# Optimization experiments

Hardware: AMD Instinct MI355X
Metric: run time of the kernel (lower is better)

## Reference

```python
import jax, jax.numpy as jnp
import numpy as np

NE, NPROC, E, D = 50000, 25000, 200000, 128
L, T = 3, 4  # layers, edge types: 0:e->e, 1:e->p, 2:p->p, 3:p->e


def setup_inputs() -> dict:
    key = jax.random.key(0)
    ks = jax.random.split(key, 17)
    s = 1.0 / np.sqrt(D)
    return {
        'x_elem': jax.random.normal(ks[0], (NE, D), jnp.float32),
        'x_proc': jax.random.normal(ks[1], (NPROC, D), jnp.float32),
        'W_src': jax.random.normal(ks[2], (L, T, D, D), jnp.float32) * s,
        'W_dst': jax.random.normal(ks[3], (L, T, D, D), jnp.float32) * s,
        'att_src': jax.random.normal(ks[4], (L, T, D), jnp.float32) * s,
        'att_dst': jax.random.normal(ks[5], (L, T, D), jnp.float32) * s,
        'bias': jax.random.normal(ks[6], (L, T, D), jnp.float32) * 0.01,
        'lin_W': jax.random.normal(ks[7], (D, 2), jnp.float32) * s,
        'lin_b': jnp.zeros((2,), jnp.float32),
        'ee_src': jax.random.randint(ks[8], (E,), 0, NE),
        'ee_dst': jax.random.randint(ks[9], (E,), 0, NE),
        'ep_src': jax.random.randint(ks[10], (E,), 0, NE),
        'ep_dst': jax.random.randint(ks[11], (E,), 0, NPROC),
        'pp_src': jax.random.randint(ks[12], (E,), 0, NPROC),
        'pp_dst': jax.random.randint(ks[13], (E,), 0, NPROC),
        'pe_src': jax.random.randint(ks[14], (E,), 0, NPROC),
        'pe_dst': jax.random.randint(ks[15], (E,), 0, NE),
    }


def _gat(x_s, x_d, src, dst, n_dst, Ws, Wd, a_s, a_d, b):
    # one GATConv (heads=1, negative_slope=0 -> relu, no self loops)
    hs = x_s @ Ws                       # [Ns, D]
    hd = x_d @ Wd                       # [Nd, D]
    es = hs @ a_s                       # [Ns]
    ed = hd @ a_d                       # [Nd]
    logit = jax.nn.relu(es[src] + ed[dst])              # [E]
    m = jax.ops.segment_max(logit, dst, num_segments=n_dst)
    m = jnp.where(jnp.isfinite(m), m, 0.0)              # empty segments
    w = jnp.exp(logit - m[dst])
    denom = jax.ops.segment_sum(w, dst, num_segments=n_dst)
    alpha = w / jnp.maximum(denom[dst], 1e-16)          # edge softmax per dst
    out = jax.ops.segment_sum(alpha[:, None] * hs[src], dst, num_segments=n_dst)
    return out + b


def reference(x_elem, x_proc, W_src, W_dst, att_src, att_dst, bias, lin_W, lin_b,
              ee_src, ee_dst, ep_src, ep_dst, pp_src, pp_dst, pe_src, pe_dst):
    xe, xp = x_elem, x_proc
    for l in range(L):
        ee = _gat(xe, xe, ee_src, ee_dst, NE, W_src[l, 0], W_dst[l, 0], att_src[l, 0], att_dst[l, 0], bias[l, 0])
        ep = _gat(xe, xp, ep_src, ep_dst, NPROC, W_src[l, 1], W_dst[l, 1], att_src[l, 1], att_dst[l, 1], bias[l, 1])
        pp = _gat(xp, xp, pp_src, pp_dst, NPROC, W_src[l, 2], W_dst[l, 2], att_src[l, 2], att_dst[l, 2], bias[l, 2])
        pe = _gat(xp, xe, pe_src, pe_dst, NE, W_src[l, 3], W_dst[l, 3], att_src[l, 3], att_dst[l, 3], bias[l, 3])
        xe = ee + pe   # to_hetero aggr='sum' per destination node type
        xp = ep + pp
    x = jnp.concatenate([xe, xp], axis=0) @ lin_W + lin_b  # G_aggr
    return x.mean(axis=0)  # [2]
```

## Files before the change

kernel.cpp:

```cpp
#include <hip/hip_runtime.h>

#define NE_N 50000
#define NP_N 25000
#define E_N 200000
#define DIM 128
#define LOG2E 1.4426950408889634f
#define NREP 1024

typedef __attribute__((ext_vector_type(8))) short short8;
typedef __attribute__((ext_vector_type(4))) float f32x4;

static __device__ __forceinline__ ushort f2bf(float f) {
  unsigned x = __float_as_uint(f);
  return (ushort)((x + 0x7fffu + ((x >> 16) & 1u)) >> 16);
}
static __device__ __forceinline__ float bf2f(ushort u) {
  return __uint_as_float(((unsigned)u) << 16);
}

#define SU_CW 12
#define SU_V 6
#define SU_H 3128
__global__ __launch_bounds__(256) void setup_fused(
    const float* __restrict__ W_src, const float* __restrict__ W_dst,
    const float* __restrict__ att_dst, ushort* __restrict__ WbT,
    float* __restrict__ vec, const int* __restrict__ d0,
    const int* __restrict__ d1, const int* __restrict__ d2,
    const int* __restrict__ d3, int* __restrict__ c0, int* __restrict__ c1,
    int* __restrict__ c2, int* __restrict__ c3, ushort* __restrict__ rk0,
    ushort* __restrict__ rk1, ushort* __restrict__ rk2,
    ushort* __restrict__ rk3) {
  int blk = blockIdx.x;
  int tid = threadIdx.x;
  if (blk < SU_CW) {
    const float* src = W_src + (size_t)blk * DIM * DIM;
    ushort* dst = WbT + (size_t)blk * DIM * DIM;
    for (int i = tid; i < DIM * DIM; i += 256) {
      int k = i >> 7, n = i & 127;
      dst[n * DIM + k] = f2bf(src[i]);
    }
  } else if (blk < SU_CW + SU_V) {
    int b = blk - SU_CW;
    int lt = b * 2 + (tid >> 7);
    int i = tid & 127;
    const float* Wd = W_dst + (size_t)lt * DIM * DIM;
    const float* ad = att_dst + lt * DIM;
    float s = 0.f;
#pragma unroll 8
    for (int j = 0; j < DIM; j++) s += Wd[i * DIM + j] * ad[j];
    vec[lt * DIM + i] = s;
  } else {
    int b = blk - SU_CW - SU_V;
    int ty = b / 782;
    int e = (b % 782) * 256 + tid;
    if (e >= E_N) return;
    const int* dst = ty == 0 ? d0 : ty == 1 ? d1 : ty == 2 ? d2 : d3;
    int* cnt = ty == 0 ? c0 : ty == 1 ? c1 : ty == 2 ? c2 : c3;
    ushort* rk = ty == 0 ? rk0 : ty == 1 ? rk1 : ty == 2 ? rk2 : rk3;
    rk[e] = (ushort)atomicAdd(&cnt[dst[e]], 1);
  }
}

__global__ __launch_bounds__(256) void scanA_k(
    const int* __restrict__ c0, const int* __restrict__ c1,
    const int* __restrict__ c2, const int* __restrict__ c3,
    int* __restrict__ part) {
  int ty = blockIdx.y;
  const int* cnt = ty == 0 ? c0 : ty == 1 ? c1 : ty == 2 ? c2 : c3;
  int n = (ty == 0 || ty == 3) ? NE_N : NP_N;
  int nblk = (n + 1023) >> 10;
  if ((int)blockIdx.x >= nblk) return;
  int base = blockIdx.x * 1024 + threadIdx.x * 4;
  int s = 0;
#pragma unroll
  for (int j = 0; j < 4; j++) s += (base + j < n) ? cnt[base + j] : 0;
  int lane = threadIdx.x & 63, wid = threadIdx.x >> 6;
#pragma unroll
  for (int off = 32; off > 0; off >>= 1) s += __shfl_xor(s, off, 64);
  __shared__ int ws4[4];
  if (lane == 0) ws4[wid] = s;
  __syncthreads();
  if (threadIdx.x == 0)
    part[ty * 64 + blockIdx.x] = ws4[0] + ws4[1] + ws4[2] + ws4[3];
}

__global__ __launch_bounds__(256) void scanBC_k(
    const int* __restrict__ c0, const int* __restrict__ c1,
    const int* __restrict__ c2, const int* __restrict__ c3,
    int* __restrict__ r0, int* __restrict__ r1, int* __restrict__ r2,
    int* __restrict__ r3, const int* __restrict__ part) {
  int ty = blockIdx.y;
  int bx = blockIdx.x;
  const int* cnt = ty == 0 ? c0 : ty == 1 ? c1 : ty == 2 ? c2 : c3;
  int* rp = ty == 0 ? r0 : ty == 1 ? r1 : ty == 2 ? r2 : r3;
  int n = (ty == 0 || ty == 3) ? NE_N : NP_N;
  int nblk = (n + 1023) >> 10;
  if (bx >= nblk) return;

  __shared__ int s_excl;
  if (threadIdx.x < 64) {
    int pl = threadIdx.x;
    int v = (pl < nblk) ? part[ty * 64 + pl] : 0;
    int sc = v;
#pragma unroll
    for (int off = 1; off < 64; off <<= 1) {
      int t = __shfl_up(sc, off, 64);
      if (pl >= off) sc += t;
    }
    if (pl == bx) s_excl = sc - v;
  }
  if (bx == 0 && threadIdx.x == 0) rp[n] = E_N;
  __syncthreads();

  int base = bx * 1024 + threadIdx.x * 4;
  int v[4];
#pragma unroll
  for (int j = 0; j < 4; j++) v[j] = (base + j < n) ? cnt[base + j] : 0;
  int s = v[0] + v[1] + v[2] + v[3];
  int lane = threadIdx.x & 63, wid = threadIdx.x >> 6;
  int sc = s;
#pragma unroll
  for (int off = 1; off < 64; off <<= 1) {
    int t = __shfl_up(sc, off, 64);
    if (lane >= off) sc += t;
  }
  __shared__ int ws4[4];
  if (lane == 63) ws4[wid] = sc;
  __syncthreads();
  int wbase = 0;
  for (int w = 0; w < wid; w++) wbase += ws4[w];
  int p = s_excl + wbase + sc - s;
#pragma unroll
  for (int j = 0; j < 4; j++) {
    if (base + j < n) rp[base + j] = p;
    p += v[j];
  }
}

#define EBLK ((NE_N + 127) / 128)
#define PBLK ((NP_N + 127) / 128)
#define GEMM_BLK (EBLK + PBLK)
#define FILL_BLK ((E_N + 511) / 512)

template <bool FP32>
static __device__ __forceinline__ void gemm_body(
    int blk, const void* __restrict__ xev, const void* __restrict__ xpv,
    const ushort* __restrict__ WbT, const float* __restrict__ att,
    const float* __restrict__ vec, int l, unsigned char* __restrict__ hsE0,
    unsigned char* __restrict__ hsE1, unsigned char* __restrict__ hsP3,
    unsigned char* __restrict__ hsP2, float* __restrict__ esE0,
    float* __restrict__ esE1, float* __restrict__ esP3,
    float* __restrict__ esP2, float* __restrict__ edEA,
    float* __restrict__ edEB, float* __restrict__ edPA,
    float* __restrict__ edPB) {
  const void* xb;
  const ushort *W0T, *W1T;
  const float *a0, *a1, *dv0, *dv1;
  unsigned char *hs0, *hs1;
  float *es0, *es1, *edA, *edB;
  int N, rbase;
  if (blk < EBLK) {
    xb = xev; N = NE_N; rbase = blk * 128;
    W0T = WbT + (size_t)(l * 4 + 0) * DIM * DIM;
    W1T = WbT + (size_t)(l * 4 + 1) * DIM * DIM;
    a0 = att + (l * 4 + 0) * DIM; a1 = att + (l * 4 + 1) * DIM;
    dv0 = vec + (l * 4 + 0) * DIM; dv1 = vec + (l * 4 + 3) * DIM;
    hs0 = hsE0; hs1 = hsE1; es0 = esE0; es1 = esE1;
    edA = edEA; edB = edEB;
  } else {
    blk -= EBLK; xb = xpv; N = NP_N; rbase = blk * 128;
    W0T = WbT + (size_t)(l * 4 + 3) * DIM * DIM;
    W1T = WbT + (size_t)(l * 4 + 2) * DIM * DIM;
    a0 = att + (l * 4 + 3) * DIM; a1 = att + (l * 4 + 2) * DIM;
    dv0 = vec + (l * 4 + 1) * DIM; dv1 = vec + (l * 4 + 2) * DIM;
    hs0 = hsP3; hs1 = hsP2; es0 = esP3; es1 = esP2;
    edA = edPA; edB = edPB;
  }

  const int wave = threadIdx.x >> 6;
  const int lane = threadIdx.x & 63;
  const int m = lane & 15, quad = lane >> 4;
  const int row0 = rbase + wave * 16;
  int rowA = row0 + m;
  if (rowA >= N) rowA = N - 1;

  float4 xraw[8];
  short8 xvv[4];
  if (FP32) {
    const float* xf32 = (const float*)xb + (size_t)rowA * DIM + quad * 8;
#pragma unroll
    for (int k0 = 0; k0 < 4; k0++) {
      xraw[2 * k0] = *(const float4*)(xf32 + k0 * 32);
      xraw[2 * k0 + 1] = *(const float4*)(xf32 + k0 * 32 + 4);
    }
  } else {
    const ushort* xb16 = (const ushort*)xb + (size_t)rowA * DIM + quad * 8;
#pragma unroll
    for (int k0 = 0; k0 < 4; k0++)
      xvv[k0] = *(const short8*)(xb16 + k0 * 32);
  }

  __shared__ short8 wlds[4096];
  {
    const int i15 = lane & 15, i4 = lane >> 4;
#pragma unroll
    for (int r = 0; r < 8; r++) {
      const int g = r * 8 + wave;
      const int set = g >> 5, k0 = (g >> 3) & 3, f = g & 7;
      const ushort* WT = set ? W1T : W0T;
      wlds[g * 64 + lane] = *(const short8*)(
          WT + (size_t)(f * 16 + i15) * DIM + k0 * 32 + i4 * 8);
    }
  }
  __syncthreads();
  if (row0 >= N) return;

  float edp0 = 0.f, edp1 = 0.f;
#pragma unroll
  for (int k0 = 0; k0 < 4; k0++) {
    float xf[8];
    if (FP32) {
      float4 f0 = xraw[2 * k0], f1 = xraw[2 * k0 + 1];
      xf[0] = f0.x; xf[1] = f0.y; xf[2] = f0.z; xf[3] = f0.w;
      xf[4] = f1.x; xf[5] = f1.y; xf[6] = f1.z; xf[7] = f1.w;
      short8 xv;
#pragma unroll
      for (int j = 0; j < 8; j++) xv[j] = (short)f2bf(xf[j]);
      xvv[k0] = xv;
    } else {
#pragma unroll
      for (int j = 0; j < 8; j++) xf[j] = bf2f((ushort)xvv[k0][j]);
    }
    int off = k0 * 32 + quad * 8;
    float4 vA0 = *(const float4*)&dv0[off];
    float4 vA1 = *(const float4*)&dv0[off + 4];
    float4 vB0 = *(const float4*)&dv1[off];
    float4 vB1 = *(const float4*)&dv1[off + 4];
    edp0 += xf[0] * vA0.x + xf[1] * vA0.y + xf[2] * vA0.z + xf[3] * vA0.w +
            xf[4] * vA1.x + xf[5] * vA1.y + xf[6] * vA1.z + xf[7] * vA1.w;
    edp1 += xf[0] * vB0.x + xf[1] * vB0.y + xf[2] * vB0.z + xf[3] * vB0.w +
            xf[4] * vB1.x + xf[5] * vB1.y + xf[6] * vB1.z + xf[7] * vB1.w;
  }

  f32x4 acc0[8], acc1[8];
#pragma unroll
  for (int f = 0; f < 8; f++) {
    acc0[f] = (f32x4){0.f, 0.f, 0.f, 0.f};
    acc1[f] = (f32x4){0.f, 0.f, 0.f, 0.f};
  }
#pragma unroll
  for (int k0 = 0; k0 < 4; k0++) {
    const short8 xv = xvv[k0];
#pragma unroll
    for (int f = 0; f < 8; f++) {
      acc0[f] = __builtin_amdgcn_mfma_f32_16x16x32_bf16(
          wlds[(k0 * 8 + f) * 64 + lane], xv, acc0[f], 0, 0, 0);
      acc1[f] = __builtin_amdgcn_mfma_f32_16x16x32_bf16(
          wlds[2048 + (k0 * 8 + f) * 64 + lane], xv, acc1[f], 0, 0, 0);
    }
  }

  const int row = row0 + m;
  edp0 += __shfl_xor(edp0, 16, 64);
  edp0 += __shfl_xor(edp0, 32, 64);
  edp1 += __shfl_xor(edp1, 16, 64);
  edp1 += __shfl_xor(edp1, 32, 64);
  if (quad == 0 && row < N) {
    edA[row] = edp0 * LOG2E;
    edB[row] = edp1 * LOG2E;
  }

#pragma unroll
  for (int set = 0; set < 2; set++) {
    f32x4* acc = set ? acc1 : acc0;
    const float* as = set ? a1 : a0;
    float* es = set ? es1 : es0;
    unsigned char* hs = set ? hs1 : hs0;

    float esum = 0.f;
#pragma unroll
    for (int f = 0; f < 8; f++) {
      float4 av = *(const float4*)&as[f * 16 + quad * 4];
      esum += acc[f][0] * av.x + acc[f][1] * av.y + acc[f][2] * av.z +
              acc[f][3] * av.w;
    }
    esum += __shfl_xor(esum, 16, 64);
    esum += __shfl_xor(esum, 32, 64);
    if (quad == 0 && row < N) es[row] = esum * LOG2E;

    if (row < N) {
#pragma unroll
      for (int f = 0; f < 8; f++) {
        int w = __builtin_amdgcn_cvt_pk_fp8_f32(acc[f][0], acc[f][1], 0, false);
        w = __builtin_amdgcn_cvt_pk_fp8_f32(acc[f][2], acc[f][3], w, true);
        *(unsigned*)&hs[(size_t)row * DIM + f * 16 + quad * 4] = (unsigned)w;
      }
    }
  }
}

__global__ __launch_bounds__(512, 4) void gemm_k(
    const ushort* __restrict__ xe, const ushort* __restrict__ xp,
    const ushort* __restrict__ WbT, const float* __restrict__ att,
    const float* __restrict__ vec, int l, unsigned char* __restrict__ hsE0,
    unsigned char* __restrict__ hsE1, unsigned char* __restrict__ hsP3,
    unsigned char* __restrict__ hsP2, float* __restrict__ esE0,
    float* __restrict__ esE1, float* __restrict__ esP3,
    float* __restrict__ esP2, float* __restrict__ edEA,
    float* __restrict__ edEB, float* __restrict__ edPA,
    float* __restrict__ edPB) {
  gemm_body<false>(blockIdx.x, xe, xp, WbT, att, vec, l, hsE0, hsE1, hsP3,
                   hsP2, esE0, esE1, esP3, esP2, edEA, edEB, edPA, edPB);
}

__global__ __launch_bounds__(512, 4) void fill_gemm0_k(
    const float* __restrict__ xe, const float* __restrict__ xp,
    const ushort* __restrict__ WbT, const float* __restrict__ att,
    const float* __restrict__ vec, unsigned char* __restrict__ hsE0,
    unsigned char* __restrict__ hsE1, unsigned char* __restrict__ hsP3,
    unsigned char* __restrict__ hsP2, float* __restrict__ esE0,
    float* __restrict__ esE1, float* __restrict__ esP3,
    float* __restrict__ esP2, float* __restrict__ edEA,
    float* __restrict__ edEB, float* __restrict__ edPA,
    float* __restrict__ edPB, const int* __restrict__ s0,
    const int* __restrict__ s1, const int* __restrict__ s2,
    const int* __restrict__ s3, const int* __restrict__ d0,
    const int* __restrict__ d1, const int* __restrict__ d2,
    const int* __restrict__ d3, const ushort* __restrict__ rk0,
    const ushort* __restrict__ rk1, const ushort* __restrict__ rk2,
    const ushort* __restrict__ rk3, const int* __restrict__ r0,
    const int* __restrict__ r1, const int* __restrict__ r2,
    const int* __restrict__ r3, ushort* __restrict__ o0,
    ushort* __restrict__ o1, ushort* __restrict__ o2,
    ushort* __restrict__ o3) {
  int blk = blockIdx.x;
  if (blk < GEMM_BLK) {
    gemm_body<true>(blk, xe, xp, WbT, att, vec, 0, hsE0, hsE1, hsP3, hsP2,
                    esE0, esE1, esP3, esP2, edEA, edEB, edPA, edPB);
  } else {
    int b = blk - GEMM_BLK;
    int ty = b / FILL_BLK;
    int e = (b % FILL_BLK) * 512 + threadIdx.x;
    if (e >= E_N) return;
    const int* src = ty == 0 ? s0 : ty == 1 ? s1 : ty == 2 ? s2 : s3;
    const int* dst = ty == 0 ? d0 : ty == 1 ? d1 : ty == 2 ? d2 : d3;
    const ushort* rk = ty == 0 ? rk0 : ty == 1 ? rk1 : ty == 2 ? rk2 : rk3;
    const int* rp = ty == 0 ? r0 : ty == 1 ? r1 : ty == 2 ? r2 : r3;
    ushort* out = ty == 0 ? o0 : ty == 1 ? o1 : ty == 2 ? o2 : o3;
    out[rp[dst[e]] + rk[e]] = (ushort)src[e];
  }
}

__global__ __launch_bounds__(256) void gat_gather_all(
    const int* __restrict__ rp0, const ushort* __restrict__ ss0,
    const int* __restrict__ rp1, const ushort* __restrict__ ss1,
    const int* __restrict__ rp2, const ushort* __restrict__ ss2,
    const int* __restrict__ rp3, const ushort* __restrict__ ss3,
    const float* __restrict__ esE0, const unsigned char* __restrict__ hsE0,
    const float* __restrict__ esE1, const unsigned char* __restrict__ hsE1,
    const float* __restrict__ esP3, const unsigned char* __restrict__ hsP3,
    const float* __restrict__ esP2, const unsigned char* __restrict__ hsP2,
    const float* __restrict__ edEA, const float* __restrict__ edEB,
    const float* __restrict__ edPA, const float* __restrict__ edPB,
    const float* __restrict__ bias, int l, ushort* __restrict__ outxe,
    ushort* __restrict__ outxp, int to_csum, float* __restrict__ csum_rep) {
  const int wid = (blockIdx.x * 256 + threadIdx.x) >> 6;
  const int lane = threadIdx.x & 63;
  const int slot = lane >> 3, sub = lane & 7;
  const int half = slot >> 2;
  const int hslot = slot & 3;
  const bool active = wid < NE_N + NP_N;

  float v0 = 0.f, v1 = 0.f;
  const float *b0 = bias, *b1 = bias;
  ushort* outb = outxe;
  int node = 0;

  if (active) {
    const int *rpA, *rpB;
    const ushort *ssA, *ssB;
    const float *esA, *esB;
    const unsigned char *hsA, *hsB;
    const float *edA, *edB;
    if (wid < NE_N) {
      node = wid;
      rpA = rp0; ssA = ss0; esA = esE0; hsA = hsE0;
      rpB = rp3; ssB = ss3; esB = esP3; hsB = hsP3;
      edA = edEA; edB = edEB;
      b0 = bias + (l * 4 + 0) * DIM; b1 = bias + (l * 4 + 3) * DIM;
      outb = outxe;
    } else {
      node = wid - NE_N;
      rpA = rp1; ssA = ss1; esA = esE1; hsA = hsE1;
      rpB = rp2; ssB = ss2; esB = esP2; hsB = hsP2;
      edA = edPA; edB = edPB;
      b0 = bias + (l * 4 + 1) * DIM; b1 = bias + (l * 4 + 2) * DIM;
      outb = outxp;
    }

    const int* rp = half ? rpB : rpA;
    const ushort* ss = half ? ssB : ssA;
    const float* es = half ? esB : esA;
    const unsigned char* hs = half ? hsB : hsA;
    const float edv = half ? edB[node] : edA[node];
    const int beg = rp[node], end = rp[node + 1];

    float acc[16];
#pragma unroll
    for (int j = 0; j < 16; j++) acc[j] = 0.f;
    float sw = 0.f;

    for (int e = beg + hslot; e < end; e += 4) {
      int s = ss[e];
      float w = exp2f(fmaxf(es[s] + edv, 0.f));
      sw += w;
      uint4 h = *(const uint4*)&hs[(size_t)s * DIM + sub * 16];
      auto p0 = __builtin_amdgcn_cvt_pk_f32_fp8((int)h.x, false);
      auto p1 = __builtin_amdgcn_cvt_pk_f32_fp8((int)h.x, true);
      auto p2 = __builtin_amdgcn_cvt_pk_f32_fp8((int)h.y, false);
      auto p3 = __builtin_amdgcn_cvt_pk_f32_fp8((int)h.y, true);
      auto p4 = __builtin_amdgcn_cvt_pk_f32_fp8((int)h.z, false);
      auto p5 = __builtin_amdgcn_cvt_pk_f32_fp8((int)h.z, true);
      auto p6 = __builtin_amdgcn_cvt_pk_f32_fp8((int)h.w, false);
      auto p7 = __builtin_amdgcn_cvt_pk_f32_fp8((int)h.w, true);
      acc[0] += w * p0[0];  acc[1] += w * p0[1];
      acc[2] += w * p1[0];  acc[3] += w * p1[1];
      acc[4] += w * p2[0];  acc[5] += w * p2[1];
      acc[6] += w * p3[0];  acc[7] += w * p3[1];
      acc[8] += w * p4[0];  acc[9] += w * p4[1];
      acc[10] += w * p5[0]; acc[11] += w * p5[1];
      acc[12] += w * p6[0]; acc[13] += w * p6[1];
      acc[14] += w * p7[0]; acc[15] += w * p7[1];
    }

    sw += __shfl_xor(sw, 8, 64);
    sw += __shfl_xor(sw, 16, 64);
    const float inv = 1.f / fmaxf(sw, 1e-16f);

    float res[16];
#pragma unroll
    for (int j = 0; j < 16; j++) res[j] = acc[j] * inv;

#pragma unroll
    for (int j = 0; j < 16; j++) {
      res[j] += __shfl_xor(res[j], 8, 64);
      res[j] += __shfl_xor(res[j], 16, 64);
      res[j] += __shfl_xor(res[j], 32, 64);
    }
    v0 = res[slot * 2];
    v1 = res[slot * 2 + 1];
  }

  const int d = sub * 16 + slot * 2;
  if (to_csum) {
    __shared__ float lsum[4][DIM];
    const int wv = threadIdx.x >> 6;
    lsum[wv][d] = v0;
    lsum[wv][d + 1] = v1;
    __syncthreads();
    if (threadIdx.x < DIM) {
      float s = lsum[0][threadIdx.x] + lsum[1][threadIdx.x] +
                lsum[2][threadIdx.x] + lsum[3][threadIdx.x];
      float* rep = csum_rep + (size_t)(blockIdx.x & (NREP - 1)) * DIM;
      unsafeAtomicAdd(&rep[threadIdx.x], s);
    }
  } else if (active) {
    float2 bb0 = *(const float2*)&b0[d];
    float2 bb1 = *(const float2*)&b1[d];
    ushort2 o;
    o.x = f2bf(v0 + bb0.x + bb1.x);
    o.y = f2bf(v1 + bb0.y + bb1.y);
    *(ushort2*)&outb[(size_t)node * DIM + d] = o;
  }
}

__global__ __launch_bounds__(512) void final_proj(
    const float* __restrict__ csum_rep, const float* __restrict__ bias,
    const float* __restrict__ lin_W, const float* __restrict__ lin_b,
    float* __restrict__ out) {
  __shared__ float parts[4][DIM];
  __shared__ float col[DIM];
  const int k = threadIdx.x & 127;
  const int pt = threadIdx.x >> 7;
  float s = 0.f;
#pragma unroll 8
  for (int r = pt * (NREP / 4); r < (pt + 1) * (NREP / 4); r++)
    s += csum_rep[(size_t)r * DIM + k];
  parts[pt][k] = s;
  __syncthreads();
  if (threadIdx.x < DIM) {
    const float* bE0 = bias + (2 * 4 + 0) * DIM;
    const float* bE1 = bias + (2 * 4 + 3) * DIM;
    const float* bP0 = bias + (2 * 4 + 1) * DIM;
    const float* bP1 = bias + (2 * 4 + 2) * DIM;
    col[k] = parts[0][k] + parts[1][k] + parts[2][k] + parts[3][k] +
             (float)NE_N * (bE0[k] + bE1[k]) +
             (float)NP_N * (bP0[k] + bP1[k]);
  }
  __syncthreads();
  if (threadIdx.x < 2) {
    float acc = 0.f;
#pragma unroll 8
    for (int j = 0; j < DIM; j++) acc += col[j] * lin_W[j * 2 + threadIdx.x];
    out[threadIdx.x] = acc / (float)(NE_N + NP_N) + lin_b[threadIdx.x];
  }
}

extern "C" void kernel_launch(void* const* d_in, const int* in_sizes, int n_in,
                              void* d_out, int out_size, void* d_ws,
                              size_t ws_size, hipStream_t stream) {
  const float* x_elem  = (const float*)d_in[0];
  const float* x_proc  = (const float*)d_in[1];
  const float* W_src   = (const float*)d_in[2];
  const float* W_dst   = (const float*)d_in[3];
  const float* att_src = (const float*)d_in[4];
  const float* att_dst = (const float*)d_in[5];
  const float* bias    = (const float*)d_in[6];
  const float* lin_W   = (const float*)d_in[7];
  const float* lin_b   = (const float*)d_in[8];
  const int* esrc[4] = {(const int*)d_in[9],  (const int*)d_in[11],
                        (const int*)d_in[13], (const int*)d_in[15]};
  const int* edst[4] = {(const int*)d_in[10], (const int*)d_in[12],
                        (const int*)d_in[14], (const int*)d_in[16]};

  char* p = (char*)d_ws;
  ushort* xe_bf[2]; ushort* xp_bf[2];
  xe_bf[0] = (ushort*)p; p += (size_t)NE_N * DIM * 2;
  xe_bf[1] = (ushort*)p; p += (size_t)NE_N * DIM * 2;
  xp_bf[0] = (ushort*)p; p += (size_t)NP_N * DIM * 2;
  xp_bf[1] = (ushort*)p; p += (size_t)NP_N * DIM * 2;
  unsigned char* hsE0 = (unsigned char*)p; p += (size_t)NE_N * DIM;
  unsigned char* hsE1 = (unsigned char*)p; p += (size_t)NE_N * DIM;
  unsigned char* hsP3 = (unsigned char*)p; p += (size_t)NP_N * DIM;
  unsigned char* hsP2 = (unsigned char*)p; p += (size_t)NP_N * DIM;
  ushort* WbT = (ushort*)p; p += (size_t)12 * DIM * DIM * 2;
  float* esE0 = (float*)p; p += (size_t)NE_N * 4;
  float* esE1 = (float*)p; p += (size_t)NE_N * 4;
  float* esP3 = (float*)p; p += (size_t)NP_N * 4;
  float* esP2 = (float*)p; p += (size_t)NP_N * 4;
  float* edEA = (float*)p; p += (size_t)NE_N * 4;
  float* edEB = (float*)p; p += (size_t)NE_N * 4;
  float* edPA = (float*)p; p += (size_t)NP_N * 4;
  float* edPB = (float*)p; p += (size_t)NP_N * 4;
  float* vec = (float*)p; p += 12 * DIM * 4;
  int* parti = (int*)p; p += 4 * 64 * 4;
  int* cnt[4];
  for (int t = 0; t < 4; t++) { cnt[t] = (int*)p; p += (NE_N + 4) * 4; }
  float* csum_rep = (float*)p; p += (size_t)NREP * DIM * 4;
  int* rp[4];
  for (int t = 0; t < 4; t++) { rp[t] = (int*)p; p += (NE_N + 4) * 4; }
  ushort* ssrc[4];
  for (int t = 0; t < 4; t++) { ssrc[t] = (ushort*)p; p += (size_t)E_N * 2; }
  ushort* rank[4];
  for (int t = 0; t < 4; t++) { rank[t] = (ushort*)p; p += (size_t)E_N * 2; }

  hipMemsetAsync(cnt[0], 0,
                 4 * (NE_N + 4) * sizeof(int) + (size_t)NREP * DIM * sizeof(float),
                 stream);

  setup_fused<<<SU_CW + SU_V + SU_H, 256, 0, stream>>>(
      W_src, W_dst, att_dst, WbT, vec, edst[0], edst[1], edst[2], edst[3],
      cnt[0], cnt[1], cnt[2], cnt[3], rank[0], rank[1], rank[2], rank[3]);

  scanA_k<<<dim3(49, 4), 256, 0, stream>>>(cnt[0], cnt[1], cnt[2], cnt[3],
                                           parti);
  scanBC_k<<<dim3(49, 4), 256, 0, stream>>>(cnt[0], cnt[1], cnt[2], cnt[3],
                                            rp[0], rp[1], rp[2], rp[3], parti);

  fill_gemm0_k<<<GEMM_BLK + 4 * FILL_BLK, 512, 0, stream>>>(
      x_elem, x_proc, WbT, att_src, vec, hsE0, hsE1, hsP3, hsP2, esE0, esE1,
      esP3, esP2, edEA, edEB, edPA, edPB, esrc[0], esrc[1], esrc[2], esrc[3],
      edst[0], edst[1], edst[2], edst[3], rank[0], rank[1], rank[2], rank[3],
      rp[0], rp[1], rp[2], rp[3], ssrc[0], ssrc[1], ssrc[2], ssrc[3]);

  int c = 0;
  for (int l = 0; l < 3; l++) {
    if (l > 0) {
      gemm_k<<<GEMM_BLK, 512, 0, stream>>>(
          xe_bf[c], xp_bf[c], WbT, att_src, vec, l, hsE0, hsE1, hsP3, hsP2,
          esE0, esE1, esP3, esP2, edEA, edEB, edPA, edPB);
    }
    int to_csum = (l == 2) ? 1 : 0;
    gat_gather_all<<<(NE_N + NP_N) / 4, 256, 0, stream>>>(
        rp[0], ssrc[0], rp[1], ssrc[1], rp[2], ssrc[2], rp[3], ssrc[3], esE0,
        hsE0, esE1, hsE1, esP3, hsP3, esP2, hsP2, edEA, edEB, edPA, edPB,
        bias, l, xe_bf[1 - c], xp_bf[1 - c], to_csum, csum_rep);
    c = 1 - c;
  }

  final_proj<<<1, 512, 0, stream>>>(csum_rep, bias, lin_W, lin_b,
                                    (float*)d_out);
}
```

Measured before the change: 412.4 us.

## Overlap layer-0 GEMM with edge histogram, interleave blocks, split fill kernel

Moves the atomic degree-histogram and rank computation out of the setup kernel and into the layer-0 GEMM launch, so the GEMM and the histogram run concurrently. Histogram blocks are spread evenly among GEMM blocks by proportional index mapping, which mixes compute-bound and atomic-bound blocks on the GPU. The CSR fill becomes its own small kernel after the scans. The setup kernel now only handles weight conversion, and the GEMM0 output no longer waits on the scans. The cost is one extra launch.

```diff
diff --git a/kernel.cpp b/kernel.cpp
--- a/kernel.cpp
+++ b/kernel.cpp
@@ -20,16 +20,10 @@
 
 #define SU_CW 12
 #define SU_V 6
-#define SU_H 3128
-__global__ __launch_bounds__(256) void setup_fused(
+__global__ __launch_bounds__(256) void setup_w(
     const float* __restrict__ W_src, const float* __restrict__ W_dst,
     const float* __restrict__ att_dst, ushort* __restrict__ WbT,
-    float* __restrict__ vec, const int* __restrict__ d0,
-    const int* __restrict__ d1, const int* __restrict__ d2,
-    const int* __restrict__ d3, int* __restrict__ c0, int* __restrict__ c1,
-    int* __restrict__ c2, int* __restrict__ c3, ushort* __restrict__ rk0,
-    ushort* __restrict__ rk1, ushort* __restrict__ rk2,
-    ushort* __restrict__ rk3) {
+    float* __restrict__ vec) {
   int blk = blockIdx.x;
   int tid = threadIdx.x;
   if (blk < SU_CW) {
@@ -39,7 +33,7 @@
       int k = i >> 7, n = i & 127;
       dst[n * DIM + k] = f2bf(src[i]);
     }
-  } else if (blk < SU_CW + SU_V) {
+  } else {
     int b = blk - SU_CW;
     int lt = b * 2 + (tid >> 7);
     int i = tid & 127;
@@ -49,15 +43,6 @@
 #pragma unroll 8
     for (int j = 0; j < DIM; j++) s += Wd[i * DIM + j] * ad[j];
     vec[lt * DIM + i] = s;
-  } else {
-    int b = blk - SU_CW - SU_V;
-    int ty = b / 782;
-    int e = (b % 782) * 256 + tid;
-    if (e >= E_N) return;
-    const int* dst = ty == 0 ? d0 : ty == 1 ? d1 : ty == 2 ? d2 : d3;
-    int* cnt = ty == 0 ? c0 : ty == 1 ? c1 : ty == 2 ? c2 : c3;
-    ushort* rk = ty == 0 ? rk0 : ty == 1 ? rk1 : ty == 2 ? rk2 : rk3;
-    rk[e] = (ushort)atomicAdd(&cnt[dst[e]], 1);
   }
 }
 
@@ -140,7 +125,8 @@
 #define EBLK ((NE_N + 127) / 128)
 #define PBLK ((NP_N + 127) / 128)
 #define GEMM_BLK (EBLK + PBLK)
-#define FILL_BLK ((E_N + 511) / 512)
+#define HIST_BLK ((E_N + 511) / 512)
+#define HG_TOT (GEMM_BLK + 4 * HIST_BLK)
 
 template <bool FP32>
 static __device__ __forceinline__ void gemm_body(
@@ -313,7 +299,7 @@
                    hsP2, esE0, esE1, esP3, esP2, edEA, edEB, edPA, edPB);
 }
 
-__global__ __launch_bounds__(512, 4) void fill_gemm0_k(
+__global__ __launch_bounds__(512, 4) void hist_gemm0_k(
     const float* __restrict__ xe, const float* __restrict__ xp,
     const ushort* __restrict__ WbT, const float* __restrict__ att,
     const float* __restrict__ vec, unsigned char* __restrict__ hsE0,
@@ -322,33 +308,51 @@
     float* __restrict__ esE1, float* __restrict__ esP3,
     float* __restrict__ esP2, float* __restrict__ edEA,
     float* __restrict__ edEB, float* __restrict__ edPA,
-    float* __restrict__ edPB, const int* __restrict__ s0,
-    const int* __restrict__ s1, const int* __restrict__ s2,
-    const int* __restrict__ s3, const int* __restrict__ d0,
+    float* __restrict__ edPB, const int* __restrict__ d0,
     const int* __restrict__ d1, const int* __restrict__ d2,
-    const int* __restrict__ d3, const ushort* __restrict__ rk0,
-    const ushort* __restrict__ rk1, const ushort* __restrict__ rk2,
-    const ushort* __restrict__ rk3, const int* __restrict__ r0,
-    const int* __restrict__ r1, const int* __restrict__ r2,
-    const int* __restrict__ r3, ushort* __restrict__ o0,
-    ushort* __restrict__ o1, ushort* __restrict__ o2,
-    ushort* __restrict__ o3) {
-  int blk = blockIdx.x;
-  if (blk < GEMM_BLK) {
-    gemm_body<true>(blk, xe, xp, WbT, att, vec, 0, hsE0, hsE1, hsP3, hsP2,
+    const int* __restrict__ d3, int* __restrict__ c0, int* __restrict__ c1,
+    int* __restrict__ c2, int* __restrict__ c3, ushort* __restrict__ rk0,
+    ushort* __restrict__ rk1, ushort* __restrict__ rk2,
+    ushort* __restrict__ rk3) {
+  const int blk = blockIdx.x;
+  const int q0 = (blk * GEMM_BLK) / HG_TOT;
+  const int q1 = ((blk + 1) * GEMM_BLK) / HG_TOT;
+  if (q1 > q0) {
+    gemm_body<true>(q0, xe, xp, WbT, att, vec, 0, hsE0, hsE1, hsP3, hsP2,
                     esE0, esE1, esP3, esP2, edEA, edEB, edPA, edPB);
   } else {
-    int b = blk - GEMM_BLK;
-    int ty = b / FILL_BLK;
-    int e = (b % FILL_BLK) * 512 + threadIdx.x;
+    const int hb = blk - q0;
+    const int ty = hb / HIST_BLK;
+    const int e = (hb % HIST_BLK) * 512 + threadIdx.x;
     if (e >= E_N) return;
-    const int* src = ty == 0 ? s0 : ty == 1 ? s1 : ty == 2 ? s2 : s3;
     const int* dst = ty == 0 ? d0 : ty == 1 ? d1 : ty == 2 ? d2 : d3;
-    const ushort* rk = ty == 0 ? rk0 : ty == 1 ? rk1 : ty == 2 ? rk2 : rk3;
-    const int* rp = ty == 0 ? r0 : ty == 1 ? r1 : ty == 2 ? r2 : r3;
-    ushort* out = ty == 0 ? o0 : ty == 1 ? o1 : ty == 2 ? o2 : o3;
-    out[rp[dst[e]] + rk[e]] = (ushort)src[e];
-  }
+    int* cnt = ty == 0 ? c0 : ty == 1 ? c1 : ty == 2 ? c2 : c3;
+    ushort* rk = ty == 0 ? rk0 : ty == 1 ? rk1 : ty == 2 ? rk2 : rk3;
+    rk[e] = (ushort)atomicAdd(&cnt[dst[e]], 1);
+  }
+}
+
+__global__ __launch_bounds__(512) void fill_k(
+    const int* __restrict__ s0, const int* __restrict__ s1,
+    const int* __restrict__ s2, const int* __restrict__ s3,
+    const int* __restrict__ d0, const int* __restrict__ d1,
+    const int* __restrict__ d2, const int* __restrict__ d3,
+    const ushort* __restrict__ rk0, const ushort* __restrict__ rk1,
+    const ushort* __restrict__ rk2, const ushort* __restrict__ rk3,
+    const int* __restrict__ r0, const int* __restrict__ r1,
+    const int* __restrict__ r2, const int* __restrict__ r3,
+    ushort* __restrict__ o0, ushort* __restrict__ o1,
+    ushort* __restrict__ o2, ushort* __restrict__ o3) {
+  int b = blockIdx.x;
+  int ty = b / HIST_BLK;
+  int e = (b % HIST_BLK) * 512 + threadIdx.x;
+  if (e >= E_N) return;
+  const int* src = ty == 0 ? s0 : ty == 1 ? s1 : ty == 2 ? s2 : s3;
+  const int* dst = ty == 0 ? d0 : ty == 1 ? d1 : ty == 2 ? d2 : d3;
+  const ushort* rk = ty == 0 ? rk0 : ty == 1 ? rk1 : ty == 2 ? rk2 : rk3;
+  const int* rp = ty == 0 ? r0 : ty == 1 ? r1 : ty == 2 ? r2 : r3;
+  ushort* out = ty == 0 ? o0 : ty == 1 ? o1 : ty == 2 ? o2 : o3;
+  out[rp[dst[e]] + rk[e]] = (ushort)src[e];
 }
 
 __global__ __launch_bounds__(256) void gat_gather_all(
@@ -558,8 +562,11 @@
                  4 * (NE_N + 4) * sizeof(int) + (size_t)NREP * DIM * sizeof(float),
                  stream);
 
-  setup_fused<<<SU_CW + SU_V + SU_H, 256, 0, stream>>>(
-      W_src, W_dst, att_dst, WbT, vec, edst[0], edst[1], edst[2], edst[3],
+  setup_w<<<SU_CW + SU_V, 256, 0, stream>>>(W_src, W_dst, att_dst, WbT, vec);
+
+  hist_gemm0_k<<<HG_TOT, 512, 0, stream>>>(
+      x_elem, x_proc, WbT, att_src, vec, hsE0, hsE1, hsP3, hsP2, esE0, esE1,
+      esP3, esP2, edEA, edEB, edPA, edPB, edst[0], edst[1], edst[2], edst[3],
       cnt[0], cnt[1], cnt[2], cnt[3], rank[0], rank[1], rank[2], rank[3]);
 
   scanA_k<<<dim3(49, 4), 256, 0, stream>>>(cnt[0], cnt[1], cnt[2], cnt[3],
@@ -567,11 +574,10 @@
   scanBC_k<<<dim3(49, 4), 256, 0, stream>>>(cnt[0], cnt[1], cnt[2], cnt[3],
                                             rp[0], rp[1], rp[2], rp[3], parti);
 
-  fill_gemm0_k<<<GEMM_BLK + 4 * FILL_BLK, 512, 0, stream>>>(
-      x_elem, x_proc, WbT, att_src, vec, hsE0, hsE1, hsP3, hsP2, esE0, esE1,
-      esP3, esP2, edEA, edEB, edPA, edPB, esrc[0], esrc[1], esrc[2], esrc[3],
-      edst[0], edst[1], edst[2], edst[3], rank[0], rank[1], rank[2], rank[3],
-      rp[0], rp[1], rp[2], rp[3], ssrc[0], ssrc[1], ssrc[2], ssrc[3]);
+  fill_k<<<4 * HIST_BLK, 512, 0, stream>>>(
+      esrc[0], esrc[1], esrc[2], esrc[3], edst[0], edst[1], edst[2], edst[3],
+      rank[0], rank[1], rank[2], rank[3], rp[0], rp[1], rp[2], rp[3],
+      ssrc[0], ssrc[1], ssrc[2], ssrc[3]);
 
   int c = 0;
   for (int l = 0; l < 3; l++) {
```

Result: no change. 410.6 us (-0.4%).

## Replace global atomic degree counting with chunked LDS hash histograms

Applied to the files above, without the earlier changes.

Each of 32 edge chunks per edge type now counts destination degrees in a shared-memory open-addressing hash table, writing local ranks and a per-node, per-chunk count table. The first scan kernel prefix-sums each node's 32 chunk counts in place to obtain totals. The fill step adds the chunk offset to the row pointer and local rank. Fill and GEMM blocks in the fused kernel are also interleaved rather than placed back to back. The goal is to remove contended global atomics, at the cost of a 32-entry-per-node count table (extra memset and scan traffic) and hash-probe work in LDS.

```diff
diff --git a/kernel.cpp b/kernel.cpp
--- a/kernel.cpp
+++ b/kernel.cpp
@@ -7,6 +7,10 @@
 #define LOG2E 1.4426950408889634f
 #define NREP 1024
 
+#define NCHK 32
+#define CHK_E (E_N / NCHK)
+#define TBL 16384
+
 typedef __attribute__((ext_vector_type(8))) short short8;
 typedef __attribute__((ext_vector_type(4))) float f32x4;
 
@@ -18,62 +22,102 @@
   return __uint_as_float(((unsigned)u) << 16);
 }
 
-#define SU_CW 12
-#define SU_V 6
-#define SU_H 3128
-__global__ __launch_bounds__(256) void setup_fused(
+#define HIST_BLKS (4 * NCHK)
+#define HS_TOT (HIST_BLKS + 12 + 3)
+__global__ __launch_bounds__(512) void hist_setup_k(
     const float* __restrict__ W_src, const float* __restrict__ W_dst,
     const float* __restrict__ att_dst, ushort* __restrict__ WbT,
     float* __restrict__ vec, const int* __restrict__ d0,
     const int* __restrict__ d1, const int* __restrict__ d2,
-    const int* __restrict__ d3, int* __restrict__ c0, int* __restrict__ c1,
-    int* __restrict__ c2, int* __restrict__ c3, ushort* __restrict__ rk0,
+    const int* __restrict__ d3, ushort* __restrict__ h0,
+    ushort* __restrict__ h1, ushort* __restrict__ h2,
+    ushort* __restrict__ h3, ushort* __restrict__ rk0,
     ushort* __restrict__ rk1, ushort* __restrict__ rk2,
     ushort* __restrict__ rk3) {
-  int blk = blockIdx.x;
-  int tid = threadIdx.x;
-  if (blk < SU_CW) {
-    const float* src = W_src + (size_t)blk * DIM * DIM;
-    ushort* dst = WbT + (size_t)blk * DIM * DIM;
-    for (int i = tid; i < DIM * DIM; i += 256) {
+  __shared__ int keys[TBL];
+  __shared__ int cnts[TBL];
+  const int blk = blockIdx.x;
+  const int tid = threadIdx.x;
+  if (blk < HIST_BLKS) {
+    const int ty = blk >> 5, c = blk & (NCHK - 1);
+    const int* dst = ty == 0 ? d0 : ty == 1 ? d1 : ty == 2 ? d2 : d3;
+    ushort* h = ty == 0 ? h0 : ty == 1 ? h1 : ty == 2 ? h2 : h3;
+    ushort* rk = ty == 0 ? rk0 : ty == 1 ? rk1 : ty == 2 ? rk2 : rk3;
+    for (int i = tid; i < TBL; i += 512) { keys[i] = -1; cnts[i] = 0; }
+    __syncthreads();
+    const int base = c * CHK_E;
+    for (int i = tid; i < CHK_E; i += 512) {
+      const int e = base + i;
+      const int d = dst[e];
+      unsigned hsh = ((unsigned)d * 2654435761u) >> 18;
+      hsh &= (TBL - 1);
+      int lr;
+      while (true) {
+        int prev = atomicCAS(&keys[hsh], -1, d);
+        if (prev == -1 || prev == d) { lr = atomicAdd(&cnts[hsh], 1); break; }
+        hsh = (hsh + 1) & (TBL - 1);
+      }
+      rk[e] = (ushort)lr;
+    }
+    __syncthreads();
+    for (int i = tid; i < TBL; i += 512) {
+      int k = keys[i];
+      if (k >= 0) h[(size_t)k * NCHK + c] = (ushort)cnts[i];
+    }
+  } else if (blk < HIST_BLKS + 12) {
+    const int w = blk - HIST_BLKS;
+    const float* src = W_src + (size_t)w * DIM * DIM;
+    ushort* dstw = WbT + (size_t)w * DIM * DIM;
+    for (int i = tid; i < DIM * DIM; i += 512) {
       int k = i >> 7, n = i & 127;
-      dst[n * DIM + k] = f2bf(src[i]);
-    }
-  } else if (blk < SU_CW + SU_V) {
-    int b = blk - SU_CW;
-    int lt = b * 2 + (tid >> 7);
-    int i = tid & 127;
+      dstw[n * DIM + k] = f2bf(src[i]);
+    }
+  } else {
+    const int b = blk - HIST_BLKS - 12;
+    const int lt = b * 4 + (tid >> 7);
+    const int i = tid & 127;
     const float* Wd = W_dst + (size_t)lt * DIM * DIM;
     const float* ad = att_dst + lt * DIM;
     float s = 0.f;
 #pragma unroll 8
     for (int j = 0; j < DIM; j++) s += Wd[i * DIM + j] * ad[j];
     vec[lt * DIM + i] = s;
-  } else {
-    int b = blk - SU_CW - SU_V;
-    int ty = b / 782;
-    int e = (b % 782) * 256 + tid;
-    if (e >= E_N) return;
-    const int* dst = ty == 0 ? d0 : ty == 1 ? d1 : ty == 2 ? d2 : d3;
-    int* cnt = ty == 0 ? c0 : ty == 1 ? c1 : ty == 2 ? c2 : c3;
-    ushort* rk = ty == 0 ? rk0 : ty == 1 ? rk1 : ty == 2 ? rk2 : rk3;
-    rk[e] = (ushort)atomicAdd(&cnt[dst[e]], 1);
   }
 }
 
 __global__ __launch_bounds__(256) void scanA_k(
-    const int* __restrict__ c0, const int* __restrict__ c1,
-    const int* __restrict__ c2, const int* __restrict__ c3,
+    ushort* __restrict__ h0, ushort* __restrict__ h1,
+    ushort* __restrict__ h2, ushort* __restrict__ h3, int* __restrict__ c0,
+    int* __restrict__ c1, int* __restrict__ c2, int* __restrict__ c3,
     int* __restrict__ part) {
   int ty = blockIdx.y;
-  const int* cnt = ty == 0 ? c0 : ty == 1 ? c1 : ty == 2 ? c2 : c3;
+  ushort* h = ty == 0 ? h0 : ty == 1 ? h1 : ty == 2 ? h2 : h3;
+  int* cnt = ty == 0 ? c0 : ty == 1 ? c1 : ty == 2 ? c2 : c3;
   int n = (ty == 0 || ty == 3) ? NE_N : NP_N;
   int nblk = (n + 1023) >> 10;
   if ((int)blockIdx.x >= nblk) return;
   int base = blockIdx.x * 1024 + threadIdx.x * 4;
   int s = 0;
 #pragma unroll
-  for (int j = 0; j < 4; j++) s += (base + j < n) ? cnt[base + j] : 0;
+  for (int j = 0; j < 4; j++) {
+    int node = base + j;
+    if (node < n) {
+      uint4* hp = (uint4*)(h + (size_t)node * NCHK);
+      uint4 a[4];
+      a[0] = hp[0]; a[1] = hp[1]; a[2] = hp[2]; a[3] = hp[3];
+      unsigned* w = (unsigned*)a;
+      int run = 0;
+#pragma unroll
+      for (int k = 0; k < 16; k++) {
+        unsigned lo = w[k] & 0xffffu, hi = w[k] >> 16;
+        w[k] = (unsigned)(run & 0xffff) | ((unsigned)((run + lo) & 0xffff) << 16);
+        run += (int)(lo + hi);
+      }
+      hp[0] = a[0]; hp[1] = a[1]; hp[2] = a[2]; hp[3] = a[3];
+      cnt[node] = run;
+      s += run;
+    }
+  }
   int lane = threadIdx.x & 63, wid = threadIdx.x >> 6;
 #pragma unroll
   for (int off = 32; off > 0; off >>= 1) s += __shfl_xor(s, off, 64);
@@ -141,6 +185,7 @@
 #define PBLK ((NP_N + 127) / 128)
 #define GEMM_BLK (EBLK + PBLK)
 #define FILL_BLK ((E_N + 511) / 512)
+#define HG2_TOT (GEMM_BLK + 4 * FILL_BLK)
 
 template <bool FP32>
 static __device__ __forceinline__ void gemm_body(
@@ -330,24 +375,32 @@
     const ushort* __restrict__ rk1, const ushort* __restrict__ rk2,
     const ushort* __restrict__ rk3, const int* __restrict__ r0,
     const int* __restrict__ r1, const int* __restrict__ r2,
-    const int* __restrict__ r3, ushort* __restrict__ o0,
+    const int* __restrict__ r3, const ushort* __restrict__ h0,
+    const ushort* __restrict__ h1, const ushort* __restrict__ h2,
+    const ushort* __restrict__ h3, ushort* __restrict__ o0,
     ushort* __restrict__ o1, ushort* __restrict__ o2,
     ushort* __restrict__ o3) {
-  int blk = blockIdx.x;
-  if (blk < GEMM_BLK) {
-    gemm_body<true>(blk, xe, xp, WbT, att, vec, 0, hsE0, hsE1, hsP3, hsP2,
+  const int blk = blockIdx.x;
+  const int q0 = (blk * GEMM_BLK) / HG2_TOT;
+  const int q1 = ((blk + 1) * GEMM_BLK) / HG2_TOT;
+  if (q1 > q0) {
+    gemm_body<true>(q0, xe, xp, WbT, att, vec, 0, hsE0, hsE1, hsP3, hsP2,
                     esE0, esE1, esP3, esP2, edEA, edEB, edPA, edPB);
   } else {
-    int b = blk - GEMM_BLK;
-    int ty = b / FILL_BLK;
-    int e = (b % FILL_BLK) * 512 + threadIdx.x;
+    const int hb = blk - q0;
+    const int ty = hb / FILL_BLK;
+    const int e = (hb % FILL_BLK) * 512 + threadIdx.x;
     if (e >= E_N) return;
     const int* src = ty == 0 ? s0 : ty == 1 ? s1 : ty == 2 ? s2 : s3;
     const int* dst = ty == 0 ? d0 : ty == 1 ? d1 : ty == 2 ? d2 : d3;
     const ushort* rk = ty == 0 ? rk0 : ty == 1 ? rk1 : ty == 2 ? rk2 : rk3;
     const int* rp = ty == 0 ? r0 : ty == 1 ? r1 : ty == 2 ? r2 : r3;
+    const ushort* ho = ty == 0 ? h0 : ty == 1 ? h1 : ty == 2 ? h2 : h3;
     ushort* out = ty == 0 ? o0 : ty == 1 ? o1 : ty == 2 ? o2 : o3;
-    out[rp[dst[e]] + rk[e]] = (ushort)src[e];
+    const int dd = dst[e];
+    const int c = e / CHK_E;
+    out[rp[dd] + (int)ho[(size_t)dd * NCHK + c] + (int)rk[e]] =
+        (ushort)src[e];
   }
 }
 
@@ -544,9 +597,14 @@
   float* edPB = (float*)p; p += (size_t)NP_N * 4;
   float* vec = (float*)p; p += 12 * DIM * 4;
   int* parti = (int*)p; p += 4 * 64 * 4;
+  float* csum_rep = (float*)p; p += (size_t)NREP * DIM * 4;
+  ushort* hh[4];
+  hh[0] = (ushort*)p; p += (size_t)NE_N * NCHK * 2;
+  hh[1] = (ushort*)p; p += (size_t)NP_N * NCHK * 2;
+  hh[2] = (ushort*)p; p += (size_t)NP_N * NCHK * 2;
+  hh[3] = (ushort*)p; p += (size_t)NE_N * NCHK * 2;
   int* cnt[4];
   for (int t = 0; t < 4; t++) { cnt[t] = (int*)p; p += (NE_N + 4) * 4; }
-  float* csum_rep = (float*)p; p += (size_t)NREP * DIM * 4;
   int* rp[4];
   for (int t = 0; t < 4; t++) { rp[t] = (int*)p; p += (NE_N + 4) * 4; }
   ushort* ssrc[4];
@@ -554,24 +612,27 @@
   ushort* rank[4];
   for (int t = 0; t < 4; t++) { rank[t] = (ushort*)p; p += (size_t)E_N * 2; }
 
-  hipMemsetAsync(cnt[0], 0,
-                 4 * (NE_N + 4) * sizeof(int) + (size_t)NREP * DIM * sizeof(float),
+  hipMemsetAsync(csum_rep, 0,
+                 (size_t)NREP * DIM * 4 +
+                     (size_t)(2 * NE_N + 2 * NP_N) * NCHK * 2,
                  stream);
 
-  setup_fused<<<SU_CW + SU_V + SU_H, 256, 0, stream>>>(
+  hist_setup_k<<<HS_TOT, 512, 0, stream>>>(
       W_src, W_dst, att_dst, WbT, vec, edst[0], edst[1], edst[2], edst[3],
-      cnt[0], cnt[1], cnt[2], cnt[3], rank[0], rank[1], rank[2], rank[3]);
-
-  scanA_k<<<dim3(49, 4), 256, 0, stream>>>(cnt[0], cnt[1], cnt[2], cnt[3],
+      hh[0], hh[1], hh[2], hh[3], rank[0], rank[1], rank[2], rank[3]);
+
+  scanA_k<<<dim3(49, 4), 256, 0, stream>>>(hh[0], hh[1], hh[2], hh[3],
+                                           cnt[0], cnt[1], cnt[2], cnt[3],
                                            parti);
   scanBC_k<<<dim3(49, 4), 256, 0, stream>>>(cnt[0], cnt[1], cnt[2], cnt[3],
                                             rp[0], rp[1], rp[2], rp[3], parti);
 
-  fill_gemm0_k<<<GEMM_BLK + 4 * FILL_BLK, 512, 0, stream>>>(
+  fill_gemm0_k<<<HG2_TOT, 512, 0, stream>>>(
       x_elem, x_proc, WbT, att_src, vec, hsE0, hsE1, hsP3, hsP2, esE0, esE1,
       esP3, esP2, edEA, edEB, edPA, edPB, esrc[0], esrc[1], esrc[2], esrc[3],
       edst[0], edst[1], edst[2], edst[3], rank[0], rank[1], rank[2], rank[3],
-      rp[0], rp[1], rp[2], rp[3], ssrc[0], ssrc[1], ssrc[2], ssrc[3]);
+      rp[0], rp[1], rp[2], rp[3], hh[0], hh[1], hh[2], hh[3],
+      ssrc[0], ssrc[1], ssrc[2], ssrc[3]);
 
   int c = 0;
   for (int l = 0; l < 3; l++) {
```

Result: faster. 401.7 us (-2.6%).
